# Kernel tuning notes

Hardware: AMD Instinct MI355X
Metric: run time of the kernel (lower is better)

Reference implementation:

```python
import jax, jax.numpy as jnp
import numpy as np

B, C, H, W = 8, 256, 48, 48
G = 32  # num_groups
EPS = 1e-5


def setup_inputs() -> dict:
    key = jax.random.key(0)
    ks = jax.random.split(key, 9)
    s = 0.02
    return {
        "input": jax.random.normal(ks[0], (B, C, H, W), dtype=jnp.float32),
        "Wq": jax.random.normal(ks[1], (C, C), dtype=jnp.float32) * s,
        "bq": jnp.zeros((C,), dtype=jnp.float32),
        "Wk": jax.random.normal(ks[2], (C, C), dtype=jnp.float32) * s,
        "bk": jnp.zeros((C,), dtype=jnp.float32),
        "Wv": jax.random.normal(ks[3], (C, C), dtype=jnp.float32) * s,
        "bv": jnp.zeros((C,), dtype=jnp.float32),
        "gn_w": jnp.ones((C,), dtype=jnp.float32),
        "gn_b": jnp.zeros((C,), dtype=jnp.float32),
    }


def _group_norm(x, w, b):
    # x: [B, C, H, W] -> normalize per (group) over (C//G, H, W)
    n, c, h, wd = x.shape
    xg = x.reshape(n, G, c // G, h, wd)
    mean = jnp.mean(xg, axis=(2, 3, 4), keepdims=True)
    var = jnp.var(xg, axis=(2, 3, 4), keepdims=True)
    xg = (xg - mean) * jax.lax.rsqrt(var + EPS)
    x = xg.reshape(n, c, h, wd)
    return x * w[None, :, None, None] + b[None, :, None, None]


def _conv1x1(x, wgt, bias):
    # 1x1 conv == per-pixel channel GEMM. wgt: [C_out, C_in]
    return jnp.einsum('bchw,oc->bohw', x, wgt) + bias[None, :, None, None]


def reference(input, Wq, bq, Wk, bk, Wv, bv, gn_w, gn_b):
    x = _group_norm(input, gn_w, gn_b)
    q = _conv1x1(x, Wq, bq)
    k = _conv1x1(x, Wk, bk)
    v = _conv1x1(x, Wv, bv)
    d = q.shape[1]
    # energy[b,h,w,h',w'] = sum_c q[b,c,h,w] * k[b,c,h',w'] / sqrt(d)
    energy = jnp.einsum('bchw,bcef->bhwef', q, k) / jnp.sqrt(jnp.float32(d))
    n, h, w2 = energy.shape[0], energy.shape[1], energy.shape[2]
    energy = jax.nn.softmax(energy.reshape(n, h, w2, h * w2), axis=-1)
    energy = energy.reshape(n, h, w2, h, w2)
    # out[b,c,h,w] = sum_{h',w'} energy[b,h,w,h',w'] * v[b,c,h',w']
    out = jnp.einsum('bhwef,bcef->bchw', energy, v)
    return out
```

## Files before the change

kernel.cpp:

```cpp
#include <hip/hip_runtime.h>
#include <math.h>

#define NB 8
#define NC 256
#define NHW 2304
#define NG 32
#define CPG 8
#define GN_EPS 1e-5f
#define ATT_SCALE 0.0625f
#define XSTR 258

typedef __bf16 bf16x8 __attribute__((ext_vector_type(8)));
typedef __bf16 bf16x4 __attribute__((ext_vector_type(4)));
typedef float f32x4 __attribute__((ext_vector_type(4)));

#define MFMA(a, b, c) __builtin_amdgcn_mfma_f32_16x16x32_bf16(a, b, c, 0, 0, 0)

__device__ __forceinline__ void async_lds16(const void* g, void* l) {
  __builtin_amdgcn_global_load_lds(
      (const __attribute__((address_space(1))) void*)g,
      (__attribute__((address_space(3))) void*)l, 16, 0, 0);
}

__global__ __launch_bounds__(256) void k_prep(
    const float* __restrict__ x, const float* __restrict__ gn_w,
    const float* __restrict__ gn_b, float* __restrict__ scale,
    float* __restrict__ shift,
    const float* __restrict__ Wq, const float* __restrict__ Wk,
    const float* __restrict__ Wv, __bf16* __restrict__ Wqb,
    __bf16* __restrict__ Wkb, __bf16* __restrict__ Wvb) {
  __shared__ float red[8];
  int blk = blockIdx.x;
  if (blk >= 256) {
    int idx = blk - 256;
    int which = idx >> 6;
    const float* src = which == 0 ? Wq : (which == 1 ? Wk : Wv);
    __bf16* dst = which == 0 ? Wqb : (which == 1 ? Wkb : Wvb);
    int i = (idx & 63) * 256 + threadIdx.x;
    float4 v = ((const float4*)src)[i];
    bf16x4 o;
    o[0] = (__bf16)v.x; o[1] = (__bf16)v.y;
    o[2] = (__bf16)v.z; o[3] = (__bf16)v.w;
    ((bf16x4*)dst)[i] = o;
    return;
  }
  const float4* base = (const float4*)(x + (size_t)blk * CPG * NHW);
  const int n4 = CPG * NHW / 4;
  float s = 0.f, ss = 0.f;
  for (int i = threadIdx.x; i < n4; i += 256) {
    float4 v = base[i];
    s  += v.x + v.y + v.z + v.w;
    ss += v.x * v.x + v.y * v.y + v.z * v.z + v.w * v.w;
  }
  for (int off = 32; off > 0; off >>= 1) {
    s  += __shfl_down(s, off);
    ss += __shfl_down(ss, off);
  }
  int wv = threadIdx.x >> 6, ln = threadIdx.x & 63;
  if (ln == 0) { red[wv] = s; red[4 + wv] = ss; }
  __syncthreads();
  if (threadIdx.x < CPG) {
    float S  = red[0] + red[1] + red[2] + red[3];
    float SS = red[4] + red[5] + red[6] + red[7];
    const float inv_n = 1.f / (float)(CPG * NHW);
    float mean = S * inv_n;
    float var  = SS * inv_n - mean * mean;
    float rstd = rsqrtf(var + GN_EPS);
    int b = blk / NG, g = blk % NG;
    int c = g * CPG + threadIdx.x;
    float sc = gn_w[c] * rstd;
    scale[b * NC + c] = sc;
    shift[b * NC + c] = gn_b[c] - mean * sc;
  }
}

__global__ __launch_bounds__(256) void k_xnT(
    const float* __restrict__ x, const float* __restrict__ scale,
    const float* __restrict__ shift, __bf16* __restrict__ xnT) {
  __shared__ __bf16 t[64 * XSTR];
  int p0 = blockIdx.x * 64;
  int b = blockIdx.y;
  int w = threadIdx.x >> 6, lane = threadIdx.x & 63;
  const float* xb = x + (size_t)b * NC * NHW;
  const float* scb = scale + b * NC;
  const float* shb = shift + b * NC;
#pragma unroll 8
  for (int i = 0; i < 64; ++i) {
    int c = i * 4 + w;
    float v = xb[(size_t)c * NHW + p0 + lane] * scb[c] + shb[c];
    t[lane * XSTR + c] = (__bf16)v;
  }
  __syncthreads();
#pragma unroll
  for (int i = 0; i < 8; ++i) {
    int row = i * 8 + w * 2 + (lane >> 5);
    int c8 = (lane & 31) * 8;
    bf16x8 v8 = *(const bf16x8*)&t[row * XSTR + c8];
    *(bf16x8*)&xnT[((size_t)b * NHW + p0 + row) * NC + c8] = v8;
  }
}

__global__ __launch_bounds__(256) void k_qkv(
    const __bf16* __restrict__ xnT,
    const __bf16* __restrict__ Wqb, const __bf16* __restrict__ Wkb,
    const __bf16* __restrict__ Wvb,
    const float* __restrict__ bq, const float* __restrict__ bk,
    const float* __restrict__ bv,
    __bf16* __restrict__ qT, __bf16* __restrict__ kT,
    __bf16* __restrict__ vbuf) {
  __shared__ __bf16 tile[9216];
  int blk = blockIdx.x;
  int b = blk & 7;
  int r = blk >> 3;
  int oq = r & 3;
  int pg = r >> 2;
  int p0 = pg * 128, o0 = oq * 64;
  int tid = threadIdx.x;
  int w = tid >> 6, lane = tid & 63;
  int col = lane & 15, quad = lane >> 4;

  const __bf16* xrow =
      xnT + ((size_t)b * NHW + p0 + w * 32 + col) * NC + quad * 8;
  bf16x8 xf[2][8];
#pragma unroll
  for (int mt = 0; mt < 2; ++mt)
#pragma unroll
    for (int ks = 0; ks < 8; ++ks)
      xf[mt][ks] = *(const bf16x8*)(xrow + (size_t)mt * 16 * NC + ks * 32);

#pragma unroll
  for (int t = 0; t < 3; ++t) {
    const __bf16* W = t == 0 ? Wqb : (t == 1 ? Wkb : Wvb);
    const float* bias = t == 0 ? bq : (t == 1 ? bk : bv);
    f32x4 acc[2][4];
#pragma unroll
    for (int mt = 0; mt < 2; ++mt)
#pragma unroll
      for (int nt = 0; nt < 4; ++nt) acc[mt][nt] = (f32x4){0.f, 0.f, 0.f, 0.f};
#pragma unroll
    for (int nt = 0; nt < 4; ++nt) {
      const __bf16* wrow = W + ((size_t)(o0 + nt * 16 + col)) * NC + quad * 8;
#pragma unroll
      for (int ks = 0; ks < 8; ++ks) {
        bf16x8 wf = *(const bf16x8*)(wrow + ks * 32);
        acc[0][nt] = MFMA(xf[0][ks], wf, acc[0][nt]);
        acc[1][nt] = MFMA(xf[1][ks], wf, acc[1][nt]);
      }
    }
    if (t > 0) __syncthreads();
    if (t < 2) {
#pragma unroll
      for (int mt = 0; mt < 2; ++mt)
#pragma unroll
        for (int nt = 0; nt < 4; ++nt) {
          float bc = bias[o0 + nt * 16 + col];
#pragma unroll
          for (int reg = 0; reg < 4; ++reg) {
            int row = w * 32 + mt * 16 + quad * 4 + reg;
            tile[row * 72 + nt * 16 + col] = (__bf16)(acc[mt][nt][reg] + bc);
          }
        }
      __syncthreads();
      __bf16* dst = t == 0 ? qT : kT;
#pragma unroll
      for (int pass = 0; pass < 4; ++pass) {
        int unit = pass * 256 + tid;
        int row = unit >> 3, ch = unit & 7;
        bf16x8 v8 = *(const bf16x8*)&tile[row * 72 + ch * 8];
        *(bf16x8*)&dst[((size_t)b * NHW + p0 + row) * NC + o0 + ch * 8] = v8;
      }
    } else {
#pragma unroll
      for (int mt = 0; mt < 2; ++mt)
#pragma unroll
        for (int nt = 0; nt < 4; ++nt) {
          float bc = bias[o0 + nt * 16 + col];
#pragma unroll
          for (int reg = 0; reg < 4; ++reg) {
            int p = w * 32 + mt * 16 + quad * 4 + reg;
            tile[(nt * 16 + col) * 136 + p] = (__bf16)(acc[mt][nt][reg] + bc);
          }
        }
      __syncthreads();
#pragma unroll
      for (int pass = 0; pass < 4; ++pass) {
        int unit = pass * 256 + tid;
        int row = unit >> 4, ch = unit & 15;
        bf16x8 v8 = *(const bf16x8*)&tile[row * 136 + ch * 8];
        *(bf16x8*)&vbuf[((size_t)b * NC + o0 + row) * NHW + p0 + ch * 8] = v8;
      }
    }
  }
}

__global__ __launch_bounds__(256, 3) void k_sexp(
    const __bf16* __restrict__ qT, const __bf16* __restrict__ kT,
    __bf16* __restrict__ P, float* __restrict__ lsum) {
  __shared__ __bf16 sk[64 * 256];
  __bf16* pt = sk;
  int blk = blockIdx.x;
  int b = blk & 7;
  int r = blk >> 3;
  int kt = r % 36;
  int qg = r / 36;
  int q0 = qg * 128, k0 = kt * 64;
  int tid = threadIdx.x;
  int w = tid >> 6, lane = tid & 63;
  int col = lane & 15, quad = lane >> 4;

  {
    int sub = lane >> 5;
    int p5 = lane & 31;
#pragma unroll
    for (int j = 0; j < 8; ++j) {
      int r0 = w * 16 + j * 2;
      int rloc = r0 + sub;
      int g = p5 ^ (rloc & 7);
      const __bf16* gp = kT + ((size_t)b * NHW + k0 + rloc) * NC + g * 8;
      async_lds16(gp, (void*)&sk[r0 * 256]);
    }
  }
  const __bf16* qrow =
      qT + ((size_t)b * NHW + q0 + w * 32 + col) * NC + quad * 8;
  bf16x8 qf[2][8];
#pragma unroll
  for (int mt = 0; mt < 2; ++mt)
#pragma unroll
    for (int ks = 0; ks < 8; ++ks)
      qf[mt][ks] = *(const bf16x8*)(qrow + (size_t)mt * 16 * NC + ks * 32);
  __syncthreads();

  f32x4 sacc[2][4];
#pragma unroll
  for (int mt = 0; mt < 2; ++mt)
#pragma unroll
    for (int nt = 0; nt < 4; ++nt) sacc[mt][nt] = (f32x4){0.f, 0.f, 0.f, 0.f};
  int c7 = col & 7;
#pragma unroll
  for (int nt = 0; nt < 4; ++nt) {
    int rrow = nt * 16 + col;
#pragma unroll
    for (int ks = 0; ks < 8; ++ks) {
      int c = ks * 4 + quad;
      bf16x8 kf = *(const bf16x8*)&sk[rrow * 256 + ((c ^ c7) << 3)];
      sacc[0][nt] = MFMA(qf[0][ks], kf, sacc[0][nt]);
      sacc[1][nt] = MFMA(qf[1][ks], kf, sacc[1][nt]);
    }
  }
#pragma unroll
  for (int mt = 0; mt < 2; ++mt)
#pragma unroll
    for (int reg = 0; reg < 4; ++reg) {
      float rs = 0.f;
#pragma unroll
      for (int nt = 0; nt < 4; ++nt) {
        float e = __expf(sacc[mt][nt][reg] * ATT_SCALE);
        sacc[mt][nt][reg] = e;
        rs += e;
      }
      rs += __shfl_xor(rs, 1);
      rs += __shfl_xor(rs, 2);
      rs += __shfl_xor(rs, 4);
      rs += __shfl_xor(rs, 8);
      if (col == 0) {
        int row = w * 32 + mt * 16 + quad * 4 + reg;
        atomicAdd(&lsum[(size_t)b * NHW + q0 + row], rs);
      }
    }
  __syncthreads();
#pragma unroll
  for (int mt = 0; mt < 2; ++mt)
#pragma unroll
    for (int nt = 0; nt < 4; ++nt)
#pragma unroll
      for (int reg = 0; reg < 4; ++reg) {
        int row = w * 32 + mt * 16 + quad * 4 + reg;
        pt[row * 72 + nt * 16 + col] = (__bf16)sacc[mt][nt][reg];
      }
  __syncthreads();
#pragma unroll
  for (int pass = 0; pass < 4; ++pass) {
    int unit = pass * 256 + tid;
    int row = unit >> 3, ch = unit & 7;
    bf16x8 v8 = *(const bf16x8*)&pt[row * 72 + ch * 8];
    *(bf16x8*)&P[((size_t)b * NHW + q0 + row) * NHW + k0 + ch * 8] = v8;
  }
}

__global__ __launch_bounds__(256, 4) void k_pv(
    const __bf16* __restrict__ P, const __bf16* __restrict__ vbuf,
    const float* __restrict__ lsum, float* __restrict__ out) {
  __shared__ __bf16 sp[3][144 * 64];
  int blk = blockIdx.x;
  int b = blk & 7;
  int r = blk >> 3;
  int cq = r & 3;
  int qg = r >> 2;
  int q0 = qg * 144;
  int tid = threadIdx.x;
  int w = tid >> 6, lane = tid & 63;
  int col = lane & 15, quad = lane >> 4;
  int c0 = cq * 64 + w * 16;

  int sub = lane >> 3;
  int gsw = (lane & 7) ^ (sub & 7);
  const __bf16* pbase = P + ((size_t)b * NHW + q0) * NHW;

  f32x4 acc[9];
#pragma unroll
  for (int nt = 0; nt < 9; ++nt) acc[nt] = (f32x4){0.f, 0.f, 0.f, 0.f};

  const __bf16* vbase =
      vbuf + ((size_t)b * NC + c0 + col) * NHW + quad * 8;
  int c7 = col & 7;

  for (int j = w; j < 18; j += 4) {
    const __bf16* gp = pbase + (size_t)(j * 8 + sub) * NHW + gsw * 8;
    async_lds16(gp, (void*)&sp[0][j * 512]);
  }
  for (int it = 0; it < 36; ++it) {
    const __bf16* buf = sp[it % 3];
    if (it < 35) {
      __bf16* nbuf = sp[(it + 1) % 3];
      const __bf16* pn = pbase + (size_t)(it + 1) * 64;
      for (int j = w; j < 18; j += 4) {
        const __bf16* gp = pn + (size_t)(j * 8 + sub) * NHW + gsw * 8;
        async_lds16(gp, (void*)&nbuf[j * 512]);
      }
      if (w < 2)
        asm volatile("s_waitcnt vmcnt(5)\n\ts_barrier" ::: "memory");
      else
        asm volatile("s_waitcnt vmcnt(4)\n\ts_barrier" ::: "memory");
    } else {
      asm volatile("s_waitcnt vmcnt(0)\n\ts_barrier" ::: "memory");
    }
    const __bf16* vp = vbase + it * 64;
#pragma unroll
    for (int ks = 0; ks < 2; ++ks) {
      bf16x8 vf = *(const bf16x8*)(vp + ks * 32);
      int c = ks * 4 + quad;
#pragma unroll
      for (int nt = 0; nt < 9; ++nt) {
        int row = nt * 16 + col;
        bf16x8 pf = *(const bf16x8*)&buf[row * 64 + ((c ^ c7) << 3)];
        acc[nt] = MFMA(vf, pf, acc[nt]);
      }
    }
  }
  float* ob = out + (size_t)b * NC * NHW;
#pragma unroll
  for (int nt = 0; nt < 9; ++nt) {
    float inv = 1.f / lsum[(size_t)b * NHW + q0 + nt * 16 + col];
#pragma unroll
    for (int reg = 0; reg < 4; ++reg) {
      int c = c0 + quad * 4 + reg;
      ob[(size_t)c * NHW + q0 + nt * 16 + col] = acc[nt][reg] * inv;
    }
  }
}

extern "C" void kernel_launch(void* const* d_in, const int* in_sizes, int n_in,
                              void* d_out, int out_size, void* d_ws,
                              size_t ws_size, hipStream_t stream) {
  const float* x   = (const float*)d_in[0];
  const float* Wq  = (const float*)d_in[1];
  const float* bq  = (const float*)d_in[2];
  const float* Wk  = (const float*)d_in[3];
  const float* bk  = (const float*)d_in[4];
  const float* Wv  = (const float*)d_in[5];
  const float* bv  = (const float*)d_in[6];
  const float* gnw = (const float*)d_in[7];
  const float* gnb = (const float*)d_in[8];
  float* out = (float*)d_out;

  const size_t per = (size_t)NB * NC * NHW;
  const size_t psz = (size_t)NB * NHW * NHW * 2;
  char* wsb = (char*)d_ws;
  __bf16* qT   = (__bf16*)wsb;
  __bf16* kT   = (__bf16*)(wsb + per * 2);
  __bf16* vbuf = (__bf16*)(wsb + per * 4);
  __bf16* xnT  = (__bf16*)(wsb + per * 6);
  __bf16* P    = (__bf16*)(wsb + per * 6);
  char* tail   = wsb + per * 6 + psz;
  __bf16* Wqb  = (__bf16*)tail;
  __bf16* Wkb  = Wqb + NC * NC;
  __bf16* Wvb  = Wkb + NC * NC;
  float* scale = (float*)(Wvb + NC * NC);
  float* shift = scale + NB * NC;
  float* lsum  = shift + NB * NC;

  hipMemsetAsync(lsum, 0, (size_t)NB * NHW * sizeof(float), stream);
  hipLaunchKernelGGL(k_prep, dim3(448), dim3(256), 0, stream,
                     x, gnw, gnb, scale, shift, Wq, Wk, Wv, Wqb, Wkb, Wvb);
  hipLaunchKernelGGL(k_xnT, dim3(NHW / 64, NB), dim3(256), 0, stream,
                     x, scale, shift, xnT);
  hipLaunchKernelGGL(k_qkv, dim3(576), dim3(256), 0, stream,
                     xnT, Wqb, Wkb, Wvb, bq, bk, bv, qT, kT, vbuf);
  hipLaunchKernelGGL(k_sexp, dim3(5184), dim3(256), 0, stream,
                     qT, kT, P, lsum);
  hipLaunchKernelGGL(k_pv, dim3(512), dim3(256), 0, stream,
                     P, vbuf, lsum, out);
}
```

Baseline: 237.7 us.

## Store P in tiled blocks and rewrite PV kernel to read tiles directly

The score kernel now writes each 128x64 probability tile as one contiguous 8192-element block, staging it in LDS as fp32 and converting to bf16 during the copy-out. Occupancy is raised to 4 blocks per SM. The PV kernel drops its LDS triple-buffered async pipeline. Each block now covers 32 query rows across all 256 channels and loads P fragments straight from the contiguous tiles into registers, launched as 576 blocks. The aim is fully coalesced P traffic and a better grid split, at the cost of losing explicit prefetch overlap and reading V more times.

```diff
diff --git a/kernel.cpp b/kernel.cpp
--- a/kernel.cpp
+++ b/kernel.cpp
@@ -9,6 +9,7 @@
 #define GN_EPS 1e-5f
 #define ATT_SCALE 0.0625f
 #define XSTR 258
+#define PTSTR 68
 
 typedef __bf16 bf16x8 __attribute__((ext_vector_type(8)));
 typedef __bf16 bf16x4 __attribute__((ext_vector_type(4)));
@@ -193,11 +194,12 @@
   }
 }
 
-__global__ __launch_bounds__(256, 3) void k_sexp(
+__global__ __launch_bounds__(256, 4) void k_sexp(
     const __bf16* __restrict__ qT, const __bf16* __restrict__ kT,
     __bf16* __restrict__ P, float* __restrict__ lsum) {
-  __shared__ __bf16 sk[64 * 256];
-  __bf16* pt = sk;
+  __shared__ __align__(16) char smem[128 * PTSTR * 4];
+  __bf16* sk = (__bf16*)smem;
+  float* pt = (float*)smem;
   int blk = blockIdx.x;
   int b = blk & 7;
   int r = blk >> 3;
@@ -275,88 +277,83 @@
 #pragma unroll
       for (int reg = 0; reg < 4; ++reg) {
         int row = w * 32 + mt * 16 + quad * 4 + reg;
-        pt[row * 72 + nt * 16 + col] = (__bf16)sacc[mt][nt][reg];
+        pt[row * PTSTR + nt * 16 + col] = sacc[mt][nt][reg];
       }
   __syncthreads();
+  __bf16* dst = P + ((size_t)((b * 18 + qg) * 36 + kt)) * 8192;
 #pragma unroll
   for (int pass = 0; pass < 4; ++pass) {
     int unit = pass * 256 + tid;
     int row = unit >> 3, ch = unit & 7;
-    bf16x8 v8 = *(const bf16x8*)&pt[row * 72 + ch * 8];
-    *(bf16x8*)&P[((size_t)b * NHW + q0 + row) * NHW + k0 + ch * 8] = v8;
+    f32x4 a = *(const f32x4*)&pt[row * PTSTR + ch * 8];
+    f32x4 bqv = *(const f32x4*)&pt[row * PTSTR + ch * 8 + 4];
+    bf16x8 v8;
+    v8[0] = (__bf16)a[0]; v8[1] = (__bf16)a[1];
+    v8[2] = (__bf16)a[2]; v8[3] = (__bf16)a[3];
+    v8[4] = (__bf16)bqv[0]; v8[5] = (__bf16)bqv[1];
+    v8[6] = (__bf16)bqv[2]; v8[7] = (__bf16)bqv[3];
+    *(bf16x8*)&dst[(size_t)unit * 8] = v8;
   }
 }
 
 __global__ __launch_bounds__(256, 4) void k_pv(
     const __bf16* __restrict__ P, const __bf16* __restrict__ vbuf,
     const float* __restrict__ lsum, float* __restrict__ out) {
-  __shared__ __bf16 sp[3][144 * 64];
   int blk = blockIdx.x;
   int b = blk & 7;
-  int r = blk >> 3;
-  int cq = r & 3;
-  int qg = r >> 2;
-  int q0 = qg * 144;
+  int qb = blk >> 3;
+  int q0 = qb * 32;
+  int qg = qb >> 2, qsub = qb & 3;
   int tid = threadIdx.x;
   int w = tid >> 6, lane = tid & 63;
   int col = lane & 15, quad = lane >> 4;
-  int c0 = cq * 64 + w * 16;
-
-  int sub = lane >> 3;
-  int gsw = (lane & 7) ^ (sub & 7);
-  const __bf16* pbase = P + ((size_t)b * NHW + q0) * NHW;
-
-  f32x4 acc[9];
-#pragma unroll
-  for (int nt = 0; nt < 9; ++nt) acc[nt] = (f32x4){0.f, 0.f, 0.f, 0.f};
-
-  const __bf16* vbase =
-      vbuf + ((size_t)b * NC + c0 + col) * NHW + quad * 8;
-  int c7 = col & 7;
-
-  for (int j = w; j < 18; j += 4) {
-    const __bf16* gp = pbase + (size_t)(j * 8 + sub) * NHW + gsw * 8;
-    async_lds16(gp, (void*)&sp[0][j * 512]);
-  }
-  for (int it = 0; it < 36; ++it) {
-    const __bf16* buf = sp[it % 3];
-    if (it < 35) {
-      __bf16* nbuf = sp[(it + 1) % 3];
-      const __bf16* pn = pbase + (size_t)(it + 1) * 64;
-      for (int j = w; j < 18; j += 4) {
-        const __bf16* gp = pn + (size_t)(j * 8 + sub) * NHW + gsw * 8;
-        async_lds16(gp, (void*)&nbuf[j * 512]);
-      }
-      if (w < 2)
-        asm volatile("s_waitcnt vmcnt(5)\n\ts_barrier" ::: "memory");
-      else
-        asm volatile("s_waitcnt vmcnt(4)\n\ts_barrier" ::: "memory");
-    } else {
-      asm volatile("s_waitcnt vmcnt(0)\n\ts_barrier" ::: "memory");
-    }
-    const __bf16* vp = vbase + it * 64;
-#pragma unroll
-    for (int ks = 0; ks < 2; ++ks) {
-      bf16x8 vf = *(const bf16x8*)(vp + ks * 32);
-      int c = ks * 4 + quad;
-#pragma unroll
-      for (int nt = 0; nt < 9; ++nt) {
-        int row = nt * 16 + col;
-        bf16x8 pf = *(const bf16x8*)&buf[row * 64 + ((c ^ c7) << 3)];
-        acc[nt] = MFMA(vf, pf, acc[nt]);
-      }
-    }
-  }
-  float* ob = out + (size_t)b * NC * NHW;
-#pragma unroll
-  for (int nt = 0; nt < 9; ++nt) {
-    float inv = 1.f / lsum[(size_t)b * NHW + q0 + nt * 16 + col];
+
+  const __bf16* ptile =
+      P + ((size_t)(b * 18 + qg) * 36) * 8192 + (size_t)qsub * 2048;
+  const __bf16* vrow =
+      vbuf + ((size_t)b * NC + w * 64 + col) * NHW + quad * 8;
+
+  f32x4 acc[4][2];
+#pragma unroll
+  for (int ct = 0; ct < 4; ++ct)
+#pragma unroll
+    for (int nt = 0; nt < 2; ++nt) acc[ct][nt] = (f32x4){0.f, 0.f, 0.f, 0.f};
+
+  for (int kt = 0; kt < 36; ++kt) {
+    const __bf16* pk = ptile + (size_t)kt * 8192;
+    bf16x8 pf[2][2];
+#pragma unroll
+    for (int nt = 0; nt < 2; ++nt)
+#pragma unroll
+      for (int ks = 0; ks < 2; ++ks)
+        pf[nt][ks] =
+            *(const bf16x8*)(pk + (nt * 16 + col) * 64 + ks * 32 + quad * 8);
+    const __bf16* vk = vrow + kt * 64;
+#pragma unroll
+    for (int ct = 0; ct < 4; ++ct) {
+#pragma unroll
+      for (int ks = 0; ks < 2; ++ks) {
+        bf16x8 vf = *(const bf16x8*)(vk + (size_t)ct * 16 * NHW + ks * 32);
+#pragma unroll
+        for (int nt = 0; nt < 2; ++nt)
+          acc[ct][nt] = MFMA(vf, pf[nt][ks], acc[ct][nt]);
+      }
+    }
+  }
+  float inv[2];
+#pragma unroll
+  for (int nt = 0; nt < 2; ++nt)
+    inv[nt] = 1.f / lsum[(size_t)b * NHW + q0 + nt * 16 + col];
+  float* ob = out + (size_t)b * NC * NHW + q0;
+#pragma unroll
+  for (int ct = 0; ct < 4; ++ct)
 #pragma unroll
     for (int reg = 0; reg < 4; ++reg) {
-      int c = c0 + quad * 4 + reg;
-      ob[(size_t)c * NHW + q0 + nt * 16 + col] = acc[nt][reg] * inv;
-    }
-  }
+      int c = w * 64 + ct * 16 + quad * 4 + reg;
+#pragma unroll
+      for (int nt = 0; nt < 2; ++nt)
+        ob[(size_t)c * NHW + nt * 16 + col] = acc[ct][nt][reg] * inv[nt];
+    }
 }
 
 extern "C" void kernel_launch(void* const* d_in, const int* in_sizes, int n_in,
@@ -398,6 +395,6 @@
                      xnT, Wqb, Wkb, Wvb, bq, bk, bv, qT, kT, vbuf);
   hipLaunchKernelGGL(k_sexp, dim3(5184), dim3(256), 0, stream,
                      qT, kT, P, lsum);
-  hipLaunchKernelGGL(k_pv, dim3(512), dim3(256), 0, stream,
+  hipLaunchKernelGGL(k_pv, dim3(576), dim3(256), 0, stream,
                      P, vbuf, lsum, out);
 }
```

Measured after the change: 337.6 us. +42.0%, slower.
